# Performance work log

Hardware: AMD Instinct MI355X
Metric: run time of the kernel (lower is better)

Reference implementation:

```python
import jax, jax.numpy as jnp
import numpy as np

N = 50000        # num nodes (num_paths)
E = 1_600_000    # num edges (avg degree 32)
W = 64           # window_size -> x feature dim
H = 128          # hidden_dimension
TEMP = 1.0       # temperature


def setup_inputs() -> dict:
    key = jax.random.key(0)
    k = jax.random.split(key, 6)
    x = jax.random.normal(k[0], (N, W), dtype=jnp.float32)
    y = jax.random.normal(k[1], (N,), dtype=jnp.float32)
    edge_index = jax.random.randint(k[2], (2, E), 0, N, dtype=jnp.int32)
    w1 = jax.random.normal(k[3], (2 * W, H), dtype=jnp.float32) / np.sqrt(2 * W)
    b1 = jnp.zeros((H,), dtype=jnp.float32)
    w2 = jax.random.normal(k[4], (H, 1), dtype=jnp.float32) / np.sqrt(H)
    b2 = jnp.zeros((1,), dtype=jnp.float32)
    return {"x": x, "y": y, "edge_index": edge_index,
            "w1": w1, "b1": b1, "w2": w2, "b2": b2}


def reference(x, y, edge_index, w1, b1, w2, b2):
    src, dst = edge_index[0], edge_index[1]
    # edge-wise gather + concat: [E, 2W]
    feat = jnp.concatenate([x[src], x[dst]], axis=1)
    # attention MLP: Linear -> ReLU -> Linear
    h = jax.nn.relu(feat @ w1 + b1)          # [E, H]
    logits = (h @ w2 + b2)[:, 0] / TEMP      # [E]
    # segment softmax over destination nodes (numerically stable)
    m = jax.ops.segment_max(logits, dst, num_segments=N)      # [N]
    e = jnp.exp(logits - m[dst])                               # [E]
    denom = jax.ops.segment_sum(e, dst, num_segments=N)       # [N]
    alpha = e / denom[dst]                                     # [E]
    # weighted scatter-sum aggregation
    y_hat = jax.ops.segment_sum(y[src] * alpha, dst, num_segments=N)  # [N]
    return y_hat, alpha[:, None]
```

## Files before the change

### kernel.cpp

```cpp
#include <hip/hip_runtime.h>

#define QSCALE 44.0f

__device__ __forceinline__ unsigned short f2bf(float f) {
    unsigned u = __float_as_uint(f);
    unsigned r = (u + 0x7fffu + ((u >> 16) & 1u)) >> 16;
    return (unsigned short)r;
}
__device__ __forceinline__ float bfu(unsigned short s) {
    return __uint_as_float(((unsigned)s) << 16);
}

__device__ __forceinline__ float dot4_i8(unsigned ax, unsigned bx, const float* w) {
    float acc = 0.f;
#pragma unroll
    for (int i = 0; i < 4; ++i) {
        int va = (int)(char)(ax >> (8 * i));
        int vb = (int)(char)(bx >> (8 * i));
        acc += w[i] * (float)max(va + vb, 0);
    }
    return acc;
}

__device__ __forceinline__ float edge_dot(const uint4& a, const uint4& b, const float* w2r) {
    float acc;
    acc  = dot4_i8(a.x, b.x, w2r + 0);
    acc += dot4_i8(a.y, b.y, w2r + 4);
    acc += dot4_i8(a.z, b.z, w2r + 8);
    acc += dot4_i8(a.w, b.w, w2r + 12);
    acc += __shfl_xor(acc, 1);
    acc += __shfl_xor(acc, 2);
    acc += __shfl_xor(acc, 4);
    return acc;
}

__device__ __forceinline__ unsigned long long pack_contrib(float ev, float ys) {
    float flo = fminf(ev * 65536.f, 1.0e9f);
    float fhi = fmaxf(fminf(ys * ev * 16384.f, 1.0e9f), -1.0e9f);
    unsigned int qlo = (unsigned int)__float2int_rn(flo);
    int          qhi = __float2int_rn(fhi);
    return ((unsigned long long)(unsigned int)qhi << 32) | (unsigned long long)qlo;
}

__device__ __forceinline__ int q8(float v) {
    return __float2int_rn(fminf(fmaxf(v * QSCALE, -127.f), 127.f)) & 0xff;
}

__global__ __launch_bounds__(256) void proj_kernel(
    const float* __restrict__ x, const float* __restrict__ w1, const float* __restrict__ b1,
    unsigned char* __restrict__ P, unsigned long long* __restrict__ agg, int N)
{
    __shared__ float xs[64 * 65];
    const int t = threadIdx.x;
    const int nloc = t & 63;
    const int n = blockIdx.x * 64 + nloc;
    const int j0 = __builtin_amdgcn_readfirstlane((t >> 6) * 32);

    if (t < 64) {
        int nn = blockIdx.x * 64 + t;
        if (nn < N) agg[nn] = 0ull;
    }

    for (int i4 = t; i4 < 64 * 16; i4 += 256) {
        const int row = i4 >> 4, c4 = (i4 & 15) * 4;
        const int nn = blockIdx.x * 64 + row;
        float4 v = make_float4(0.f, 0.f, 0.f, 0.f);
        if (nn < N) v = *(const float4*)&x[(size_t)nn * 64 + c4];
        float* d = &xs[row * 65 + c4];
        d[0] = v.x; d[1] = v.y; d[2] = v.z; d[3] = v.w;
    }
    __syncthreads();

    float accA[32], accB[32];
#pragma unroll
    for (int c = 0; c < 32; ++c) { accA[c] = b1[j0 + c]; accB[c] = 0.f; }

    const float* __restrict__ xrow = &xs[nloc * 65];
    for (int k = 0; k < 64; ++k) {
        const float xv = xrow[k];
        const float* __restrict__ wa = w1 + k * 128 + j0;
        const float* __restrict__ wb = w1 + (64 + k) * 128 + j0;
#pragma unroll
        for (int c = 0; c < 32; ++c) {
            accA[c] = fmaf(xv, wa[c], accA[c]);
            accB[c] = fmaf(xv, wb[c], accB[c]);
        }
    }

    if (n < N) {
        unsigned dwA[8], dwB[8];
#pragma unroll
        for (int d = 0; d < 8; ++d) {
            dwA[d] = (unsigned)q8(accA[d * 4 + 0])
                   | ((unsigned)q8(accA[d * 4 + 1]) << 8)
                   | ((unsigned)q8(accA[d * 4 + 2]) << 16)
                   | ((unsigned)q8(accA[d * 4 + 3]) << 24);
            dwB[d] = (unsigned)q8(accB[d * 4 + 0])
                   | ((unsigned)q8(accB[d * 4 + 1]) << 8)
                   | ((unsigned)q8(accB[d * 4 + 2]) << 16)
                   | ((unsigned)q8(accB[d * 4 + 3]) << 24);
        }
        unsigned char* pA = P + (size_t)n * 256 + j0;
        unsigned char* pB = P + (size_t)n * 256 + 128 + j0;
        *(uint4*)(pA)      = make_uint4(dwA[0], dwA[1], dwA[2], dwA[3]);
        *(uint4*)(pA + 16) = make_uint4(dwA[4], dwA[5], dwA[6], dwA[7]);
        *(uint4*)(pB)      = make_uint4(dwB[0], dwB[1], dwB[2], dwB[3]);
        *(uint4*)(pB + 16) = make_uint4(dwB[4], dwB[5], dwB[6], dwB[7]);
    }
}

__global__ __launch_bounds__(256) void edge_logit_kernel(
    const unsigned char* __restrict__ P, const int* __restrict__ ei,
    const float* __restrict__ y,
    const float* __restrict__ w2, const float* __restrict__ b2,
    unsigned short* __restrict__ evh, unsigned long long* __restrict__ agg, int E)
{
    const int lane = threadIdx.x & 7;
    float w2r[16];
#pragma unroll
    for (int c = 0; c < 16; ++c) w2r[c] = w2[lane * 16 + c] * (1.0f / QSCALE);
    const float b2s = b2[0];

    const int slot = (blockIdx.x * 256 + threadIdx.x) >> 3;
    const int nslots = (gridDim.x * 256) >> 3;
    const int lo16 = lane * 16;

    for (int base = slot * 4; base < E; base += nslots * 4) {
        if (base + 3 < E) {
            const int4 s4 = *(const int4*)&ei[base];
            const int4 d4 = *(const int4*)&ei[E + base];

            const uint4 a0 = *(const uint4*)(P + (size_t)s4.x * 256 + lo16);
            const uint4 b0 = *(const uint4*)(P + (size_t)d4.x * 256 + 128 + lo16);
            const uint4 a1 = *(const uint4*)(P + (size_t)s4.y * 256 + lo16);
            const uint4 b1v = *(const uint4*)(P + (size_t)d4.y * 256 + 128 + lo16);
            const uint4 a2 = *(const uint4*)(P + (size_t)s4.z * 256 + lo16);
            const uint4 b2v = *(const uint4*)(P + (size_t)d4.z * 256 + 128 + lo16);
            const uint4 a3 = *(const uint4*)(P + (size_t)s4.w * 256 + lo16);
            const uint4 b3 = *(const uint4*)(P + (size_t)d4.w * 256 + 128 + lo16);

            const float acc0 = edge_dot(a0, b0, w2r);
            const float acc1 = edge_dot(a1, b1v, w2r);
            const float acc2 = edge_dot(a2, b2v, w2r);
            const float acc3 = edge_dot(a3, b3, w2r);

            if (lane == 0) {
                const float ys0 = y[s4.x];
                const float ys1 = y[s4.y];
                const float ys2 = y[s4.z];
                const float ys3 = y[s4.w];
                const float ev0 = __expf(acc0 + b2s);
                const float ev1 = __expf(acc1 + b2s);
                const float ev2 = __expf(acc2 + b2s);
                const float ev3 = __expf(acc3 + b2s);
                *(ushort4*)&evh[base] = make_ushort4(f2bf(ev0), f2bf(ev1), f2bf(ev2), f2bf(ev3));
                atomicAdd(&agg[d4.x], pack_contrib(ev0, ys0));
                atomicAdd(&agg[d4.y], pack_contrib(ev1, ys1));
                atomicAdd(&agg[d4.z], pack_contrib(ev2, ys2));
                atomicAdd(&agg[d4.w], pack_contrib(ev3, ys3));
            }
        } else {
            for (int e = base; e < E; ++e) {
                const int s = ei[e];
                const int d = ei[E + e];
                const uint4 a = *(const uint4*)(P + (size_t)s * 256 + lo16);
                const uint4 b = *(const uint4*)(P + (size_t)d * 256 + 128 + lo16);
                const float acc = edge_dot(a, b, w2r);
                if (lane == 0) {
                    const float ev = __expf(acc + b2s);
                    evh[e] = f2bf(ev);
                    atomicAdd(&agg[d], pack_contrib(ev, y[s]));
                }
            }
        }
    }
}

__global__ __launch_bounds__(256) void decode_alpha_kernel(
    const int* __restrict__ ei, const unsigned long long* __restrict__ agg,
    const unsigned short* __restrict__ evh, float* __restrict__ alpha,
    float* __restrict__ yhat, int N, int E)
{
    const int gtid = blockIdx.x * 256 + threadIdx.x;
    const int ntot = gridDim.x * 256;

    for (int i = gtid; i < N; i += ntot) {
        unsigned long long v = agg[i];
        unsigned int lo = (unsigned int)(v & 0xffffffffull);
        int          hi = (int)(v >> 32);
        yhat[i] = (lo != 0u) ? 4.0f * (float)hi / (float)lo : 0.f;
    }

    for (int base = gtid * 4; base < E; base += ntot * 4) {
        if (base + 3 < E) {
            const int4 d4 = *(const int4*)&ei[E + base];
            const ushort4 eh = *(const ushort4*)&evh[base];
            const unsigned int l0 = (unsigned int)(agg[d4.x] & 0xffffffffull);
            const unsigned int l1 = (unsigned int)(agg[d4.y] & 0xffffffffull);
            const unsigned int l2 = (unsigned int)(agg[d4.z] & 0xffffffffull);
            const unsigned int l3 = (unsigned int)(agg[d4.w] & 0xffffffffull);
            float4 av;
            av.x = l0 ? bfu(eh.x) * (65536.0f / (float)l0) : 0.f;
            av.y = l1 ? bfu(eh.y) * (65536.0f / (float)l1) : 0.f;
            av.z = l2 ? bfu(eh.z) * (65536.0f / (float)l2) : 0.f;
            av.w = l3 ? bfu(eh.w) * (65536.0f / (float)l3) : 0.f;
            *(float4*)&alpha[base] = av;
        } else {
            for (int e = base; e < E; ++e) {
                const unsigned int lo = (unsigned int)(agg[ei[E + e]] & 0xffffffffull);
                alpha[e] = lo ? bfu(evh[e]) * (65536.0f / (float)lo) : 0.f;
            }
        }
    }
}

extern "C" void kernel_launch(void* const* d_in, const int* in_sizes, int n_in,
                              void* d_out, int out_size, void* d_ws, size_t ws_size,
                              hipStream_t stream) {
    const float* x  = (const float*)d_in[0];
    const float* y  = (const float*)d_in[1];
    const int*   ei = (const int*)d_in[2];
    const float* w1 = (const float*)d_in[3];
    const float* b1 = (const float*)d_in[4];
    const float* w2 = (const float*)d_in[5];
    const float* b2 = (const float*)d_in[6];

    const int N = in_sizes[1];
    const int E = in_sizes[2] / 2;

    float* out   = (float*)d_out;
    float* yhat  = out;
    float* alpha = out + N;

    char* ws = (char*)d_ws;
    unsigned char* P = (unsigned char*)ws;
    const size_t Pbytes = (size_t)N * 256;
    unsigned long long* agg = (unsigned long long*)(ws + Pbytes);
    unsigned short* evh = (unsigned short*)(ws + Pbytes + (size_t)N * 8);

    proj_kernel<<<(N + 63) / 64, 256, 0, stream>>>(x, w1, b1, P, agg, N);
    edge_logit_kernel<<<2048, 256, 0, stream>>>(P, ei, y, w2, b2, evh, agg, E);
    decode_alpha_kernel<<<1600, 256, 0, stream>>>(ei, agg, evh, alpha, yhat, N, E);
}
```

Measured before the change: 198.5 us.

## Fuse edge-logit and decode kernels into one cooperative kernel with grid barrier

Merges the edge logit/atomic-accumulate phase and the alpha decode phase into a single cooperative launch of 2048 blocks, separated by a software grid barrier built on an atomic counter in workspace. This removes one kernel launch and the inter-kernel gap. The cost is an extra memset for the barrier counter, a spin-wait barrier, and forcing both phases to run at the same grid size. A fallback to the two separate kernels is kept for when occupancy is below 8 blocks per CU.

```diff
diff --git a/kernel.cpp b/kernel.cpp
--- a/kernel.cpp
+++ b/kernel.cpp
@@ -46,83 +46,34 @@
     return __float2int_rn(fminf(fmaxf(v * QSCALE, -127.f), 127.f)) & 0xff;
 }
 
-__global__ __launch_bounds__(256) void proj_kernel(
-    const float* __restrict__ x, const float* __restrict__ w1, const float* __restrict__ b1,
-    unsigned char* __restrict__ P, unsigned long long* __restrict__ agg, int N)
-{
-    __shared__ float xs[64 * 65];
-    const int t = threadIdx.x;
-    const int nloc = t & 63;
-    const int n = blockIdx.x * 64 + nloc;
-    const int j0 = __builtin_amdgcn_readfirstlane((t >> 6) * 32);
-
-    if (t < 64) {
-        int nn = blockIdx.x * 64 + t;
-        if (nn < N) agg[nn] = 0ull;
-    }
-
-    for (int i4 = t; i4 < 64 * 16; i4 += 256) {
-        const int row = i4 >> 4, c4 = (i4 & 15) * 4;
-        const int nn = blockIdx.x * 64 + row;
-        float4 v = make_float4(0.f, 0.f, 0.f, 0.f);
-        if (nn < N) v = *(const float4*)&x[(size_t)nn * 64 + c4];
-        float* d = &xs[row * 65 + c4];
-        d[0] = v.x; d[1] = v.y; d[2] = v.z; d[3] = v.w;
-    }
+__device__ __forceinline__ void grid_sync(unsigned long long* bar, int nblk) {
     __syncthreads();
-
-    float accA[32], accB[32];
-#pragma unroll
-    for (int c = 0; c < 32; ++c) { accA[c] = b1[j0 + c]; accB[c] = 0.f; }
-
-    const float* __restrict__ xrow = &xs[nloc * 65];
-    for (int k = 0; k < 64; ++k) {
-        const float xv = xrow[k];
-        const float* __restrict__ wa = w1 + k * 128 + j0;
-        const float* __restrict__ wb = w1 + (64 + k) * 128 + j0;
-#pragma unroll
-        for (int c = 0; c < 32; ++c) {
-            accA[c] = fmaf(xv, wa[c], accA[c]);
-            accB[c] = fmaf(xv, wb[c], accB[c]);
-        }
-    }
-
-    if (n < N) {
-        unsigned dwA[8], dwB[8];
-#pragma unroll
-        for (int d = 0; d < 8; ++d) {
-            dwA[d] = (unsigned)q8(accA[d * 4 + 0])
-                   | ((unsigned)q8(accA[d * 4 + 1]) << 8)
-                   | ((unsigned)q8(accA[d * 4 + 2]) << 16)
-                   | ((unsigned)q8(accA[d * 4 + 3]) << 24);
-            dwB[d] = (unsigned)q8(accB[d * 4 + 0])
-                   | ((unsigned)q8(accB[d * 4 + 1]) << 8)
-                   | ((unsigned)q8(accB[d * 4 + 2]) << 16)
-                   | ((unsigned)q8(accB[d * 4 + 3]) << 24);
-        }
-        unsigned char* pA = P + (size_t)n * 256 + j0;
-        unsigned char* pB = P + (size_t)n * 256 + 128 + j0;
-        *(uint4*)(pA)      = make_uint4(dwA[0], dwA[1], dwA[2], dwA[3]);
-        *(uint4*)(pA + 16) = make_uint4(dwA[4], dwA[5], dwA[6], dwA[7]);
-        *(uint4*)(pB)      = make_uint4(dwB[0], dwB[1], dwB[2], dwB[3]);
-        *(uint4*)(pB + 16) = make_uint4(dwB[4], dwB[5], dwB[6], dwB[7]);
-    }
-}
-
-__global__ __launch_bounds__(256) void edge_logit_kernel(
+    if (threadIdx.x == 0) {
+        __threadfence();
+        unsigned long long t = atomicAdd(bar, 1ull) + 1ull;
+        unsigned long long nb = (unsigned long long)nblk;
+        unsigned long long target = ((t + nb - 1ull) / nb) * nb;
+        while (__hip_atomic_load(bar, __ATOMIC_RELAXED, __HIP_MEMORY_SCOPE_AGENT) < target)
+            __builtin_amdgcn_s_sleep(2);
+        __threadfence();
+    }
+    __syncthreads();
+}
+
+__device__ __forceinline__ void edge_phase(
     const unsigned char* __restrict__ P, const int* __restrict__ ei,
-    const float* __restrict__ y,
-    const float* __restrict__ w2, const float* __restrict__ b2,
-    unsigned short* __restrict__ evh, unsigned long long* __restrict__ agg, int E)
-{
-    const int lane = threadIdx.x & 7;
+    const float* __restrict__ y, const float* __restrict__ w2,
+    const float* __restrict__ b2, unsigned short* __restrict__ evh,
+    unsigned long long* __restrict__ agg, int E, int gtid, int nthreads)
+{
+    const int lane = gtid & 7;
     float w2r[16];
 #pragma unroll
     for (int c = 0; c < 16; ++c) w2r[c] = w2[lane * 16 + c] * (1.0f / QSCALE);
     const float b2s = b2[0];
 
-    const int slot = (blockIdx.x * 256 + threadIdx.x) >> 3;
-    const int nslots = (gridDim.x * 256) >> 3;
+    const int slot = gtid >> 3;
+    const int nslots = nthreads >> 3;
     const int lo16 = lane * 16;
 
     for (int base = slot * 4; base < E; base += nslots * 4) {
@@ -176,14 +127,11 @@
     }
 }
 
-__global__ __launch_bounds__(256) void decode_alpha_kernel(
+__device__ __forceinline__ void decode_phase(
     const int* __restrict__ ei, const unsigned long long* __restrict__ agg,
     const unsigned short* __restrict__ evh, float* __restrict__ alpha,
-    float* __restrict__ yhat, int N, int E)
-{
-    const int gtid = blockIdx.x * 256 + threadIdx.x;
-    const int ntot = gridDim.x * 256;
-
+    float* __restrict__ yhat, int N, int E, int gtid, int ntot)
+{
     for (int i = gtid; i < N; i += ntot) {
         unsigned long long v = agg[i];
         unsigned int lo = (unsigned int)(v & 0xffffffffull);
@@ -214,6 +162,102 @@
     }
 }
 
+__global__ __launch_bounds__(256) void proj_kernel(
+    const float* __restrict__ x, const float* __restrict__ w1, const float* __restrict__ b1,
+    unsigned char* __restrict__ P, unsigned long long* __restrict__ agg, int N)
+{
+    __shared__ float xs[64 * 65];
+    const int t = threadIdx.x;
+    const int nloc = t & 63;
+    const int n = blockIdx.x * 64 + nloc;
+    const int j0 = __builtin_amdgcn_readfirstlane((t >> 6) * 32);
+
+    if (t < 64) {
+        int nn = blockIdx.x * 64 + t;
+        if (nn < N) agg[nn] = 0ull;
+    }
+
+    for (int i4 = t; i4 < 64 * 16; i4 += 256) {
+        const int row = i4 >> 4, c4 = (i4 & 15) * 4;
+        const int nn = blockIdx.x * 64 + row;
+        float4 v = make_float4(0.f, 0.f, 0.f, 0.f);
+        if (nn < N) v = *(const float4*)&x[(size_t)nn * 64 + c4];
+        float* d = &xs[row * 65 + c4];
+        d[0] = v.x; d[1] = v.y; d[2] = v.z; d[3] = v.w;
+    }
+    __syncthreads();
+
+    float accA[32], accB[32];
+#pragma unroll
+    for (int c = 0; c < 32; ++c) { accA[c] = b1[j0 + c]; accB[c] = 0.f; }
+
+    const float* __restrict__ xrow = &xs[nloc * 65];
+    for (int k = 0; k < 64; ++k) {
+        const float xv = xrow[k];
+        const float* __restrict__ wa = w1 + k * 128 + j0;
+        const float* __restrict__ wb = w1 + (64 + k) * 128 + j0;
+#pragma unroll
+        for (int c = 0; c < 32; ++c) {
+            accA[c] = fmaf(xv, wa[c], accA[c]);
+            accB[c] = fmaf(xv, wb[c], accB[c]);
+        }
+    }
+
+    if (n < N) {
+        unsigned dwA[8], dwB[8];
+#pragma unroll
+        for (int d = 0; d < 8; ++d) {
+            dwA[d] = (unsigned)q8(accA[d * 4 + 0])
+                   | ((unsigned)q8(accA[d * 4 + 1]) << 8)
+                   | ((unsigned)q8(accA[d * 4 + 2]) << 16)
+                   | ((unsigned)q8(accA[d * 4 + 3]) << 24);
+            dwB[d] = (unsigned)q8(accB[d * 4 + 0])
+                   | ((unsigned)q8(accB[d * 4 + 1]) << 8)
+                   | ((unsigned)q8(accB[d * 4 + 2]) << 16)
+                   | ((unsigned)q8(accB[d * 4 + 3]) << 24);
+        }
+        unsigned char* pA = P + (size_t)n * 256 + j0;
+        unsigned char* pB = P + (size_t)n * 256 + 128 + j0;
+        *(uint4*)(pA)      = make_uint4(dwA[0], dwA[1], dwA[2], dwA[3]);
+        *(uint4*)(pA + 16) = make_uint4(dwA[4], dwA[5], dwA[6], dwA[7]);
+        *(uint4*)(pB)      = make_uint4(dwB[0], dwB[1], dwB[2], dwB[3]);
+        *(uint4*)(pB + 16) = make_uint4(dwB[4], dwB[5], dwB[6], dwB[7]);
+    }
+}
+
+__global__ __launch_bounds__(256, 8) void edge_decode_coop_kernel(
+    const unsigned char* __restrict__ P, const int* __restrict__ ei,
+    const float* __restrict__ y, const float* __restrict__ w2,
+    const float* __restrict__ b2, unsigned short* __restrict__ evh,
+    unsigned long long* __restrict__ agg, unsigned long long* __restrict__ bar,
+    float* __restrict__ alpha, float* __restrict__ yhat, int N, int E, int nblk)
+{
+    const int gtid = blockIdx.x * 256 + threadIdx.x;
+    const int nthreads = nblk * 256;
+    edge_phase(P, ei, y, w2, b2, evh, agg, E, gtid, nthreads);
+    grid_sync(bar, nblk);
+    decode_phase(ei, agg, evh, alpha, yhat, N, E, gtid, nthreads);
+}
+
+__global__ __launch_bounds__(256) void edge_logit_kernel(
+    const unsigned char* __restrict__ P, const int* __restrict__ ei,
+    const float* __restrict__ y,
+    const float* __restrict__ w2, const float* __restrict__ b2,
+    unsigned short* __restrict__ evh, unsigned long long* __restrict__ agg, int E)
+{
+    const int gtid = blockIdx.x * 256 + threadIdx.x;
+    edge_phase(P, ei, y, w2, b2, evh, agg, E, gtid, gridDim.x * 256);
+}
+
+__global__ __launch_bounds__(256) void decode_alpha_kernel(
+    const int* __restrict__ ei, const unsigned long long* __restrict__ agg,
+    const unsigned short* __restrict__ evh, float* __restrict__ alpha,
+    float* __restrict__ yhat, int N, int E)
+{
+    const int gtid = blockIdx.x * 256 + threadIdx.x;
+    decode_phase(ei, agg, evh, alpha, yhat, N, E, gtid, gridDim.x * 256);
+}
+
 extern "C" void kernel_launch(void* const* d_in, const int* in_sizes, int n_in,
                               void* d_out, int out_size, void* d_ws, size_t ws_size,
                               hipStream_t stream) {
@@ -233,12 +277,31 @@
     float* alpha = out + N;
 
     char* ws = (char*)d_ws;
-    unsigned char* P = (unsigned char*)ws;
+    unsigned long long* bar = (unsigned long long*)ws;
+    unsigned char* P = (unsigned char*)(ws + 256);
     const size_t Pbytes = (size_t)N * 256;
-    unsigned long long* agg = (unsigned long long*)(ws + Pbytes);
-    unsigned short* evh = (unsigned short*)(ws + Pbytes + (size_t)N * 8);
+    unsigned long long* agg = (unsigned long long*)(ws + 256 + Pbytes);
+    unsigned short* evh = (unsigned short*)(ws + 256 + Pbytes + (size_t)N * 8);
 
     proj_kernel<<<(N + 63) / 64, 256, 0, stream>>>(x, w1, b1, P, agg, N);
-    edge_logit_kernel<<<2048, 256, 0, stream>>>(P, ei, y, w2, b2, evh, agg, E);
-    decode_alpha_kernel<<<1600, 256, 0, stream>>>(ei, agg, evh, alpha, yhat, N, E);
-}
+
+    static int maxBlkPerCU = -1;
+    if (maxBlkPerCU < 0) {
+        hipError_t oe = hipOccupancyMaxActiveBlocksPerMultiprocessor(
+            &maxBlkPerCU, (const void*)edge_decode_coop_kernel, 256, 0);
+        if (oe != hipSuccess || maxBlkPerCU < 1) maxBlkPerCU = 0;
+    }
+
+    if (maxBlkPerCU >= 8) {
+        int nblk = 2048;
+        hipMemsetAsync(bar, 0, 8, stream);
+        void* args[] = {(void*)&P, (void*)&ei, (void*)&y, (void*)&w2, (void*)&b2,
+                        (void*)&evh, (void*)&agg, (void*)&bar, (void*)&alpha,
+                        (void*)&yhat, (void*)&N, (void*)&E, (void*)&nblk};
+        hipLaunchCooperativeKernel((void*)edge_decode_coop_kernel,
+                                   dim3(nblk), dim3(256), args, 0, stream);
+    } else {
+        edge_logit_kernel<<<2048, 256, 0, stream>>>(P, ei, y, w2, b2, evh, agg, E);
+        decode_alpha_kernel<<<1600, 256, 0, stream>>>(ei, agg, evh, alpha, yhat, N, E);
+    }
+}
```

Measured after the change: 197.1 us. About the same (-0.7%).
